# Kernel optimization log

Hardware: AMD Instinct MI355X
Metric: run time of the kernel (lower is better)

The kernel has to match this reference:

```python
import jax, jax.numpy as jnp
import numpy as np

B, S, D, H = 4, 2048, 1024, 16
W = D // H  # head width = 64


def setup_inputs() -> dict:
    key = jax.random.key(0)
    ks = jax.random.split(key, 7)
    sc = 0.02
    return {
        "x": jax.random.normal(ks[0], (B, S, D), dtype=jnp.float32),
        "mask": jnp.ones((B, S), dtype=jnp.int32),
        "Wq": jax.random.normal(ks[1], (D, D), dtype=jnp.float32) * sc,
        "bq": jax.random.normal(ks[2], (D,), dtype=jnp.float32) * sc,
        "Wk": jax.random.normal(ks[3], (D, D), dtype=jnp.float32) * sc,
        "bk": jax.random.normal(ks[4], (D,), dtype=jnp.float32) * sc,
        "Wv": jax.random.normal(ks[5], (D, D), dtype=jnp.float32) * sc,
        "bv": jax.random.normal(ks[6], (D,), dtype=jnp.float32) * sc,
    }


def reference(x, mask, Wq, bq, Wk, bk, Wv, bv):
    # Linear projections (torch Linear: y = x @ W.T + b)
    q = x @ Wq.T + bq  # (B,S,D)
    k = x @ Wk.T + bk
    v = x @ Wv.T + bv
    # split D -> (H, W) and move heads forward: (B,H,S,W)
    def split(t):
        return t.reshape(B, S, H, W).transpose(0, 2, 1, 3)
    q, k, v = split(q), split(k), split(v)
    scale = 1.0 / np.sqrt(W).astype(np.float32)
    scores = jnp.einsum("bhsw,bhtw->bhst", q, k) * scale  # (B,H,S,S)
    m = mask[:, None, None, :].astype(scores.dtype)  # (B,1,1,S)
    scores = scores - 10000.0 * (1.0 - m)
    probs = jax.nn.softmax(scores, axis=-1)  # dropout p=0.0 -> identity
    h = jnp.einsum("bhst,bhtw->bhsw", probs, v)  # (B,H,S,W)
    h = h.transpose(0, 2, 1, 3).reshape(B, S, D)  # merge heads
    return h
```

## Files before the change

### kernel.cpp

```cpp
#include <hip/hip_runtime.h>
#include <hip/hip_bf16.h>


#define NB 4
#define NS 2048
#define ND 1024
#define NH 16
#define NW 64

typedef __bf16 bf16;
typedef __bf16 bf16x2 __attribute__((ext_vector_type(2)));
typedef __bf16 bf16x4 __attribute__((ext_vector_type(4)));
typedef __bf16 bf16x8 __attribute__((ext_vector_type(8)));
typedef float f32x4 __attribute__((ext_vector_type(4)));
typedef float f32x16 __attribute__((ext_vector_type(16)));
typedef unsigned u32x4 __attribute__((ext_vector_type(4)));

__device__ __forceinline__ void gld_lds16(const void* g, void* l) {
  __builtin_amdgcn_global_load_lds(
      (const __attribute__((address_space(1))) void*)g,
      (__attribute__((address_space(3))) void*)l, 16, 0, 0);
}

__device__ __forceinline__ unsigned pack2(float lo, float hi) {
  bf16x2 t;
  t[0] = (bf16)lo;
  t[1] = (bf16)hi;
  return __builtin_bit_cast(unsigned, t);
}

__global__ void cast_f32_bf16(const float* __restrict__ src,
                              bf16* __restrict__ dst, int n) {
  int i = (blockIdx.x * blockDim.x + threadIdx.x) * 8;
  int stride = gridDim.x * blockDim.x * 8;
  for (; i < n; i += stride) {
    float4 a = *reinterpret_cast<const float4*>(src + i);
    float4 b = *reinterpret_cast<const float4*>(src + i + 4);
    bf16x8 o;
    o[0] = (bf16)a.x; o[1] = (bf16)a.y; o[2] = (bf16)a.z; o[3] = (bf16)a.w;
    o[4] = (bf16)b.x; o[5] = (bf16)b.y; o[6] = (bf16)b.z; o[7] = (bf16)b.w;
    *reinterpret_cast<bf16x8*>(dst + i) = o;
  }
}

__global__ void cast_weights(const float* __restrict__ a,
                             const float* __restrict__ b,
                             const float* __restrict__ c,
                             bf16* __restrict__ dst) {
  const int n = ND * ND;
  const int which = blockIdx.y;
  const float* src = (which == 0) ? a : ((which == 1) ? b : c);
  bf16* d = dst + (size_t)which * n;
  int i = (blockIdx.x * blockDim.x + threadIdx.x) * 8;
  float4 u = *reinterpret_cast<const float4*>(src + i);
  float4 v = *reinterpret_cast<const float4*>(src + i + 4);
  bf16x8 o;
  o[0] = (bf16)u.x; o[1] = (bf16)u.y; o[2] = (bf16)u.z; o[3] = (bf16)u.w;
  o[4] = (bf16)v.x; o[5] = (bf16)v.y; o[6] = (bf16)v.z; o[7] = (bf16)v.w;
  *reinterpret_cast<bf16x8*>(d + i) = o;
}

__global__ void mask_to_bf16(const int* __restrict__ mask,
                             bf16* __restrict__ mb, int n) {
  int i = blockIdx.x * blockDim.x + threadIdx.x;
  if (i < n) mb[i] = (bf16)(mask[i] ? 1.0f : 0.0f);
}

__global__ __launch_bounds__(256) void proj_kernel(
    const bf16* __restrict__ xb,
    const bf16* __restrict__ wq,
    const bf16* __restrict__ wk,
    const bf16* __restrict__ wv,
    const float* __restrict__ bq,
    const float* __restrict__ bk,
    const float* __restrict__ bv,
    const int* __restrict__ mask,
    bf16* __restrict__ qh,
    bf16* __restrict__ kh,
    bf16* __restrict__ vt) {
  const int mode = blockIdx.z;
  const bf16* wmat = (mode == 0) ? wq : ((mode == 1) ? wk : wv);
  const float* bias = (mode == 0) ? bq : ((mode == 1) ? bk : bv);

  __shared__ alignas(16) bf16 a_lds[128][64];
  __shared__ alignas(16) bf16 b_lds[128][64];

  const int tid = threadIdx.x;
  const int wave = tid >> 6;
  const int lane = tid & 63;
  const int wr = wave >> 1, wc = wave & 1;
  const int m0 = blockIdx.x * 128;
  const int n0 = blockIdx.y * 128;

  f32x4 acc[4][4] = {};

  const int srow = tid >> 3;
  const int scol = (tid & 7) * 8;
  const int sw_scol = scol ^ ((srow & 7) << 3);
  const int xr = (lane & 7) << 3;
  const int lr = lane & 15;
  const int g = lane >> 4;
  const int kq = g * 8;

  for (int k0 = 0; k0 < 1024; k0 += 64) {
#pragma unroll
    for (int c = 0; c < 4; ++c) {
      int row = srow + c * 32;
      gld_lds16(xb + (size_t)(m0 + row) * 1024 + k0 + sw_scol, &a_lds[row][scol]);
      gld_lds16(wmat + (size_t)(n0 + row) * 1024 + k0 + sw_scol, &b_lds[row][scol]);
    }
    __syncthreads();
#pragma unroll
    for (int kk = 0; kk < 64; kk += 32) {
      bf16x8 af[4], bfr[4];
      const int col = (kk + kq) ^ xr;
#pragma unroll
      for (int mf = 0; mf < 4; ++mf)
        af[mf] = *reinterpret_cast<const bf16x8*>(&a_lds[wr * 64 + mf * 16 + lr][col]);
#pragma unroll
      for (int nf = 0; nf < 4; ++nf)
        bfr[nf] = *reinterpret_cast<const bf16x8*>(&b_lds[wc * 64 + nf * 16 + lr][col]);
      if (mode == 2) {
#pragma unroll
        for (int mf = 0; mf < 4; ++mf)
#pragma unroll
          for (int nf = 0; nf < 4; ++nf)
            acc[mf][nf] = __builtin_amdgcn_mfma_f32_16x16x32_bf16(af[mf], bfr[nf], acc[mf][nf], 0, 0, 0);
      } else {
#pragma unroll
        for (int nf = 0; nf < 4; ++nf)
#pragma unroll
          for (int mf = 0; mf < 4; ++mf)
            acc[nf][mf] = __builtin_amdgcn_mfma_f32_16x16x32_bf16(bfr[nf], af[mf], acc[nf][mf], 0, 0, 0);
      }
    }
    __syncthreads();
  }

  if (mode == 2) {
    float msk[4][4];
#pragma unroll
    for (int mf = 0; mf < 4; ++mf) {
      const int i0 = m0 + wr * 64 + mf * 16 + g * 4;
      const int b = i0 >> 11, s = i0 & 2047;
      const int4 mm = *reinterpret_cast<const int4*>(mask + b * NS + s);
      msk[mf][0] = mm.x ? 1.f : 0.f;
      msk[mf][1] = mm.y ? 1.f : 0.f;
      msk[mf][2] = mm.z ? 1.f : 0.f;
      msk[mf][3] = mm.w ? 1.f : 0.f;
    }
#pragma unroll
    for (int nf = 0; nf < 4; ++nf) {
      const int j = n0 + wc * 64 + nf * 16 + lr;
      const float bj = bias[j];
      const int h = j >> 6, w = j & 63;
#pragma unroll
      for (int mf = 0; mf < 4; ++mf) {
        const int i0 = m0 + wr * 64 + mf * 16 + g * 4;
        const int b = i0 >> 11, s = i0 & 2047;
        bf16x4 pk;
#pragma unroll
        for (int r = 0; r < 4; ++r)
          pk[r] = (bf16)((acc[mf][nf][r] + bj) * msk[mf][r]);
        *reinterpret_cast<bf16x4*>(&vt[(((size_t)(b * NH + h)) * NW + w) * NS + s]) = pk;
      }
    }
  } else {
    bf16* dst = (mode == 0) ? qh : kh;
    const float scl = (mode == 0) ? 0.18033688011112042f : 1.0f;
#pragma unroll
    for (int nf = 0; nf < 4; ++nf) {
      const int j0 = n0 + wc * 64 + nf * 16 + g * 4;
      const f32x4 bj = *reinterpret_cast<const f32x4*>(&bias[j0]);
      const int h = j0 >> 6, w0 = j0 & 63;
#pragma unroll
      for (int mf = 0; mf < 4; ++mf) {
        const int i = m0 + wr * 64 + mf * 16 + lr;
        const int b = i >> 11, s = i & 2047;
        bf16x4 pk;
#pragma unroll
        for (int r = 0; r < 4; ++r)
          pk[r] = (bf16)((acc[nf][mf][r] + bj[r]) * scl);
        *reinterpret_cast<bf16x4*>(&dst[(((size_t)(b * NH + h)) * NS + s) * NW + w0]) = pk;
      }
    }
  }
}

__global__ __launch_bounds__(256, 4) void attn_kernel(
    const bf16* __restrict__ qh,
    const bf16* __restrict__ kh,
    const bf16* __restrict__ vt,
    const bf16* __restrict__ mb16,
    float* __restrict__ out) {
  __shared__ alignas(16) bf16 k_lds[2][64][64];
  __shared__ alignas(16) bf16 v_lds[2][64][64];

  const int tid = threadIdx.x;
  const int wave = tid >> 6;
  const int lane = tid & 63;
  const int lq = lane & 31;
  const int hi = lane >> 5;
  const int xr = (lq & 7) << 3;

  const int p = blockIdx.x;
  const int w_id = (p & 7) * 128 + (p >> 3);
  const int bh = w_id >> 4;
  const int b = bh >> 4;
  const int q0 = (w_id & 15) * 128;
  const size_t headoff = (size_t)bh * NS * NW;

  bf16x8 qf[4];
  {
    const bf16* qp = qh + headoff + (size_t)(q0 + wave * 32 + lq) * NW + hi * 8;
#pragma unroll
    for (int m = 0; m < 4; ++m)
      qf[m] = *reinterpret_cast<const bf16x8*>(qp + m * 16);
  }

  f32x16 o0 = {}, o1 = {}, lt = {};
  const bf16* mp = mb16 + b * NS;

  const int srow = tid >> 3;
  const int scol = (tid & 7) * 8;
  const int sw_scol = scol ^ ((srow & 7) << 3);

#define STAGE(buf, kt)                                                          \
  {                                                                             \
    _Pragma("unroll") for (int c = 0; c < 2; ++c) {                             \
      const int row = srow + c * 32;                                            \
      gld_lds16(kh + headoff + (size_t)((kt) + row) * NW + sw_scol,             \
                &k_lds[buf][row][scol]);                                        \
      gld_lds16(vt + headoff + (size_t)row * NS + (kt) + sw_scol,               \
                &v_lds[buf][row][scol]);                                        \
    }                                                                           \
  }

#define EXPPACK(S, PA0, PA1)                                                    \
  {                                                                             \
    unsigned w_[8];                                                             \
    _Pragma("unroll") for (int j = 0; j < 8; ++j)                               \
        w_[j] = pack2(exp2f(S[2 * j]), exp2f(S[2 * j + 1]));                    \
    asm("v_permlane32_swap_b32 %0, %1" : "+v"(w_[0]), "+v"(w_[2]));             \
    asm("v_permlane32_swap_b32 %0, %1" : "+v"(w_[1]), "+v"(w_[3]));             \
    asm("v_permlane32_swap_b32 %0, %1" : "+v"(w_[4]), "+v"(w_[6]));             \
    asm("v_permlane32_swap_b32 %0, %1" : "+v"(w_[5]), "+v"(w_[7]));             \
    u32x4 u0 = {w_[0], w_[1], w_[2], w_[3]};                                    \
    u32x4 u1 = {w_[4], w_[5], w_[6], w_[7]};                                    \
    PA0 = __builtin_bit_cast(bf16x8, u0);                                       \
    PA1 = __builtin_bit_cast(bf16x8, u1);                                       \
  }

  STAGE(0, 0);
  __syncthreads();

  int cur = 0;
  for (int kt = 0; kt < NS; kt += 64) {
    if (kt + 64 < NS) STAGE(cur ^ 1, kt + 64);

    f32x16 s0 = {}, s1 = {};
    __builtin_amdgcn_s_setprio(1);
#pragma unroll
    for (int m = 0; m < 4; ++m) {
      const int col = (m * 16 + hi * 8) ^ xr;
      bf16x8 kf0 = *reinterpret_cast<const bf16x8*>(&k_lds[cur][lq][col]);
      s0 = __builtin_amdgcn_mfma_f32_32x32x16_bf16(kf0, qf[m], s0, 0, 0, 0);
      bf16x8 kf1 = *reinterpret_cast<const bf16x8*>(&k_lds[cur][32 + lq][col]);
      s1 = __builtin_amdgcn_mfma_f32_32x32x16_bf16(kf1, qf[m], s1, 0, 0, 0);
    }
    __builtin_amdgcn_s_setprio(0);

    bf16x8 pa0, pa1, pa2, pa3;
    EXPPACK(s0, pa0, pa1);
    EXPPACK(s1, pa2, pa3);

    const bf16* mpk = mp + kt + hi * 8;
    bf16x8 mf00 = *reinterpret_cast<const bf16x8*>(mpk);
    bf16x8 mf01 = *reinterpret_cast<const bf16x8*>(mpk + 16);
    bf16x8 mf10 = *reinterpret_cast<const bf16x8*>(mpk + 32);
    bf16x8 mf11 = *reinterpret_cast<const bf16x8*>(mpk + 48);

    __builtin_amdgcn_s_setprio(1);
    lt = __builtin_amdgcn_mfma_f32_32x32x16_bf16(pa0, mf00, lt, 0, 0, 0);
    lt = __builtin_amdgcn_mfma_f32_32x32x16_bf16(pa1, mf01, lt, 0, 0, 0);
    lt = __builtin_amdgcn_mfma_f32_32x32x16_bf16(pa2, mf10, lt, 0, 0, 0);
    lt = __builtin_amdgcn_mfma_f32_32x32x16_bf16(pa3, mf11, lt, 0, 0, 0);
#pragma unroll
    for (int G = 0; G < 2; ++G) {
      const bf16x8 a0 = G ? pa2 : pa0;
      const bf16x8 a1 = G ? pa3 : pa1;
      const int c0 = (G * 32 + hi * 8) ^ xr;
      const int c1 = (G * 32 + 16 + hi * 8) ^ xr;
      bf16x8 v00 = *reinterpret_cast<const bf16x8*>(&v_lds[cur][lq][c0]);
      o0 = __builtin_amdgcn_mfma_f32_32x32x16_bf16(a0, v00, o0, 0, 0, 0);
      bf16x8 v01 = *reinterpret_cast<const bf16x8*>(&v_lds[cur][lq][c1]);
      o0 = __builtin_amdgcn_mfma_f32_32x32x16_bf16(a1, v01, o0, 0, 0, 0);
      bf16x8 v10 = *reinterpret_cast<const bf16x8*>(&v_lds[cur][32 + lq][c0]);
      o1 = __builtin_amdgcn_mfma_f32_32x32x16_bf16(a0, v10, o1, 0, 0, 0);
      bf16x8 v11 = *reinterpret_cast<const bf16x8*>(&v_lds[cur][32 + lq][c1]);
      o1 = __builtin_amdgcn_mfma_f32_32x32x16_bf16(a1, v11, o1, 0, 0, 0);
    }
    __builtin_amdgcn_s_setprio(0);

    __syncthreads();
    cur ^= 1;
  }

  const int h = bh & 15;
  float* op = out + ((size_t)b * NS) * ND + h * NW;
#pragma unroll
  for (int r = 0; r < 16; ++r) {
    const int sq = q0 + wave * 32 + (r & 3) + 8 * (r >> 2) + 4 * hi;
    const float inv = 1.0f / lt[r];
    op[(size_t)sq * ND + lq] = o0[r] * inv;
    op[(size_t)sq * ND + 32 + lq] = o1[r] * inv;
  }
#undef STAGE
#undef EXPPACK
}

extern "C" void kernel_launch(void* const* d_in, const int* in_sizes, int n_in,
                              void* d_out, int out_size, void* d_ws, size_t ws_size,
                              hipStream_t stream) {
  const float* x = (const float*)d_in[0];
  const int* mask = (const int*)d_in[1];
  const float* Wq = (const float*)d_in[2];
  const float* bq = (const float*)d_in[3];
  const float* Wk = (const float*)d_in[4];
  const float* bk = (const float*)d_in[5];
  const float* Wv = (const float*)d_in[6];
  const float* bv = (const float*)d_in[7];
  float* out = (float*)d_out;

  char* ws = (char*)d_ws;
  bf16* wqb = (bf16*)(ws + (size_t)(0) * (1 << 20));
  bf16* wkb = (bf16*)(ws + (size_t)(2) * (1 << 20));
  bf16* wvb = (bf16*)(ws + (size_t)(4) * (1 << 20));
  bf16* qhb = (bf16*)(ws + (size_t)(6) * (1 << 20));
  bf16* khb = (bf16*)(ws + (size_t)(22) * (1 << 20));
  bf16* vtb = (bf16*)(ws + (size_t)(38) * (1 << 20));
  bf16* mb16 = (bf16*)(ws + (size_t)(54) * (1 << 20));
  bf16* xb = (bf16*)d_out;

  cast_f32_bf16<<<2048, 256, 0, stream>>>(x, xb, NB * NS * ND);
  cast_weights<<<dim3(512, 3), 256, 0, stream>>>(Wq, Wk, Wv, wqb);
  mask_to_bf16<<<32, 256, 0, stream>>>(mask, mb16, NB * NS);
  proj_kernel<<<dim3(64, 8, 3), 256, 0, stream>>>(xb, wqb, wkb, wvb, bq, bk, bv,
                                                  mask, qhb, khb, vtb);
  attn_kernel<<<1024, 256, 0, stream>>>(qhb, khb, vtb, mb16, out);
}
```

Measured before the change: 310.3 us.

## Double-buffer projection GEMM LDS, template per mode, remap blocks per XCD

The projection GEMM now double-buffers its LDS tiles, so the next K-slice's global-to-LDS loads are issued before computing on the current slice, and one barrier per iteration is removed. The kernel is templated on mode and launched three times instead of branching on blockIdx.z, and blocks are remapped so each XCD handles a contiguous group of M tiles for better L2 reuse. This doubles LDS use to 64KB per block, which may lower occupancy, and adds two extra kernel launches.

```diff
diff --git a/kernel.cpp b/kernel.cpp
--- a/kernel.cpp
+++ b/kernel.cpp
@@ -66,31 +66,25 @@
   if (i < n) mb[i] = (bf16)(mask[i] ? 1.0f : 0.0f);
 }
 
+template <int MODE>
 __global__ __launch_bounds__(256) void proj_kernel(
     const bf16* __restrict__ xb,
-    const bf16* __restrict__ wq,
-    const bf16* __restrict__ wk,
-    const bf16* __restrict__ wv,
-    const float* __restrict__ bq,
-    const float* __restrict__ bk,
-    const float* __restrict__ bv,
+    const bf16* __restrict__ wmat,
+    const float* __restrict__ bias,
     const int* __restrict__ mask,
-    bf16* __restrict__ qh,
-    bf16* __restrict__ kh,
-    bf16* __restrict__ vt) {
-  const int mode = blockIdx.z;
-  const bf16* wmat = (mode == 0) ? wq : ((mode == 1) ? wk : wv);
-  const float* bias = (mode == 0) ? bq : ((mode == 1) ? bk : bv);
-
-  __shared__ alignas(16) bf16 a_lds[128][64];
-  __shared__ alignas(16) bf16 b_lds[128][64];
+    bf16* __restrict__ dst) {
+  __shared__ alignas(16) bf16 a_lds[2][128][64];
+  __shared__ alignas(16) bf16 b_lds[2][128][64];
 
   const int tid = threadIdx.x;
   const int wave = tid >> 6;
   const int lane = tid & 63;
   const int wr = wave >> 1, wc = wave & 1;
-  const int m0 = blockIdx.x * 128;
-  const int n0 = blockIdx.y * 128;
+
+  const int p = blockIdx.x;
+  const int xcd = p & 7, q = p >> 3;
+  const int m0 = (xcd * 8 + (q & 7)) * 128;
+  const int n0 = (q >> 3) * 128;
 
   f32x4 acc[4][4] = {};
 
@@ -102,25 +96,34 @@
   const int g = lane >> 4;
   const int kq = g * 8;
 
+#define PSTAGE(buf, k0)                                                         \
+  {                                                                             \
+    _Pragma("unroll") for (int c = 0; c < 4; ++c) {                             \
+      const int row = srow + c * 32;                                            \
+      gld_lds16(xb + (size_t)(m0 + row) * 1024 + (k0) + sw_scol,                \
+                &a_lds[buf][row][scol]);                                        \
+      gld_lds16(wmat + (size_t)(n0 + row) * 1024 + (k0) + sw_scol,              \
+                &b_lds[buf][row][scol]);                                        \
+    }                                                                           \
+  }
+
+  PSTAGE(0, 0);
+  __syncthreads();
+
+  int cur = 0;
   for (int k0 = 0; k0 < 1024; k0 += 64) {
-#pragma unroll
-    for (int c = 0; c < 4; ++c) {
-      int row = srow + c * 32;
-      gld_lds16(xb + (size_t)(m0 + row) * 1024 + k0 + sw_scol, &a_lds[row][scol]);
-      gld_lds16(wmat + (size_t)(n0 + row) * 1024 + k0 + sw_scol, &b_lds[row][scol]);
-    }
-    __syncthreads();
+    if (k0 + 64 < 1024) PSTAGE(cur ^ 1, k0 + 64);
 #pragma unroll
     for (int kk = 0; kk < 64; kk += 32) {
       bf16x8 af[4], bfr[4];
       const int col = (kk + kq) ^ xr;
 #pragma unroll
       for (int mf = 0; mf < 4; ++mf)
-        af[mf] = *reinterpret_cast<const bf16x8*>(&a_lds[wr * 64 + mf * 16 + lr][col]);
+        af[mf] = *reinterpret_cast<const bf16x8*>(&a_lds[cur][wr * 64 + mf * 16 + lr][col]);
 #pragma unroll
       for (int nf = 0; nf < 4; ++nf)
-        bfr[nf] = *reinterpret_cast<const bf16x8*>(&b_lds[wc * 64 + nf * 16 + lr][col]);
-      if (mode == 2) {
+        bfr[nf] = *reinterpret_cast<const bf16x8*>(&b_lds[cur][wc * 64 + nf * 16 + lr][col]);
+      if (MODE == 2) {
 #pragma unroll
         for (int mf = 0; mf < 4; ++mf)
 #pragma unroll
@@ -135,9 +138,10 @@
       }
     }
     __syncthreads();
-  }
-
-  if (mode == 2) {
+    cur ^= 1;
+  }
+
+  if (MODE == 2) {
     float msk[4][4];
 #pragma unroll
     for (int mf = 0; mf < 4; ++mf) {
@@ -162,12 +166,11 @@
 #pragma unroll
         for (int r = 0; r < 4; ++r)
           pk[r] = (bf16)((acc[mf][nf][r] + bj) * msk[mf][r]);
-        *reinterpret_cast<bf16x4*>(&vt[(((size_t)(b * NH + h)) * NW + w) * NS + s]) = pk;
+        *reinterpret_cast<bf16x4*>(&dst[(((size_t)(b * NH + h)) * NW + w) * NS + s]) = pk;
       }
     }
   } else {
-    bf16* dst = (mode == 0) ? qh : kh;
-    const float scl = (mode == 0) ? 0.18033688011112042f : 1.0f;
+    const float scl = (MODE == 0) ? 0.18033688011112042f : 1.0f;
 #pragma unroll
     for (int nf = 0; nf < 4; ++nf) {
       const int j0 = n0 + wc * 64 + nf * 16 + g * 4;
@@ -185,6 +188,7 @@
       }
     }
   }
+#undef PSTAGE
 }
 
 __global__ __launch_bounds__(256, 4) void attn_kernel(
@@ -345,7 +349,8 @@
   cast_f32_bf16<<<2048, 256, 0, stream>>>(x, xb, NB * NS * ND);
   cast_weights<<<dim3(512, 3), 256, 0, stream>>>(Wq, Wk, Wv, wqb);
   mask_to_bf16<<<32, 256, 0, stream>>>(mask, mb16, NB * NS);
-  proj_kernel<<<dim3(64, 8, 3), 256, 0, stream>>>(xb, wqb, wkb, wvb, bq, bk, bv,
-                                                  mask, qhb, khb, vtb);
+  proj_kernel<0><<<512, 256, 0, stream>>>(xb, wqb, bq, mask, qhb);
+  proj_kernel<1><<<512, 256, 0, stream>>>(xb, wkb, bk, mask, khb);
+  proj_kernel<2><<<512, 256, 0, stream>>>(xb, wvb, bv, mask, vtb);
   attn_kernel<<<1024, 256, 0, stream>>>(qhb, khb, vtb, mb16, out);
 }
```

New measurement: 281.6 us. -9.3%, faster.

## Remap projection blocks per XCD, unify MFMA order, use fast exp2

Applied to the files above, without the earlier changes.

The projection launch changes from a 3D grid to a 1D-per-mode grid and remaps block indices so that consecutive blocks on the same XCD share weight column tiles, aiming at better L2 reuse. The V projection now uses the same MFMA operand order as Q/K, which removes the branch in the inner loop. Its transposed store becomes scalar strided bf16 writes instead of packed 4-element writes, which may cost store efficiency. The attention exp uses the hardware exp2 builtin to avoid libm range handling.

```diff
diff --git a/kernel.cpp b/kernel.cpp
--- a/kernel.cpp
+++ b/kernel.cpp
@@ -66,11 +66,9 @@
   if (i < n) mb[i] = (bf16)(mask[i] ? 1.0f : 0.0f);
 }
 
-__global__ __launch_bounds__(256) void proj_kernel(
+__global__ __launch_bounds__(256) void proj_fused(
     const bf16* __restrict__ xb,
-    const bf16* __restrict__ wq,
-    const bf16* __restrict__ wk,
-    const bf16* __restrict__ wv,
+    const bf16* __restrict__ wall,
     const float* __restrict__ bq,
     const float* __restrict__ bk,
     const float* __restrict__ bv,
@@ -78,8 +76,8 @@
     bf16* __restrict__ qh,
     bf16* __restrict__ kh,
     bf16* __restrict__ vt) {
-  const int mode = blockIdx.z;
-  const bf16* wmat = (mode == 0) ? wq : ((mode == 1) ? wk : wv);
+  const int mode = blockIdx.y;
+  const bf16* wmat = wall + (size_t)mode * ND * ND;
   const float* bias = (mode == 0) ? bq : ((mode == 1) ? bk : bv);
 
   __shared__ alignas(16) bf16 a_lds[128][64];
@@ -89,8 +87,11 @@
   const int wave = tid >> 6;
   const int lane = tid & 63;
   const int wr = wave >> 1, wc = wave & 1;
-  const int m0 = blockIdx.x * 128;
-  const int n0 = blockIdx.y * 128;
+
+  const int p = blockIdx.x;
+  const int xcd = p & 7, q = p >> 3;
+  const int m0 = (xcd * 8 + (q & 7)) * 128;
+  const int n0 = (q >> 3) * 128;
 
   f32x4 acc[4][4] = {};
 
@@ -105,7 +106,7 @@
   for (int k0 = 0; k0 < 1024; k0 += 64) {
 #pragma unroll
     for (int c = 0; c < 4; ++c) {
-      int row = srow + c * 32;
+      const int row = srow + c * 32;
       gld_lds16(xb + (size_t)(m0 + row) * 1024 + k0 + sw_scol, &a_lds[row][scol]);
       gld_lds16(wmat + (size_t)(n0 + row) * 1024 + k0 + sw_scol, &b_lds[row][scol]);
     }
@@ -120,49 +121,30 @@
 #pragma unroll
       for (int nf = 0; nf < 4; ++nf)
         bfr[nf] = *reinterpret_cast<const bf16x8*>(&b_lds[wc * 64 + nf * 16 + lr][col]);
-      if (mode == 2) {
+#pragma unroll
+      for (int nf = 0; nf < 4; ++nf)
 #pragma unroll
         for (int mf = 0; mf < 4; ++mf)
-#pragma unroll
-          for (int nf = 0; nf < 4; ++nf)
-            acc[mf][nf] = __builtin_amdgcn_mfma_f32_16x16x32_bf16(af[mf], bfr[nf], acc[mf][nf], 0, 0, 0);
-      } else {
-#pragma unroll
-        for (int nf = 0; nf < 4; ++nf)
-#pragma unroll
-          for (int mf = 0; mf < 4; ++mf)
-            acc[nf][mf] = __builtin_amdgcn_mfma_f32_16x16x32_bf16(bfr[nf], af[mf], acc[nf][mf], 0, 0, 0);
-      }
+          acc[nf][mf] = __builtin_amdgcn_mfma_f32_16x16x32_bf16(bfr[nf], af[mf], acc[nf][mf], 0, 0, 0);
     }
     __syncthreads();
   }
 
   if (mode == 2) {
-    float msk[4][4];
 #pragma unroll
     for (int mf = 0; mf < 4; ++mf) {
-      const int i0 = m0 + wr * 64 + mf * 16 + g * 4;
-      const int b = i0 >> 11, s = i0 & 2047;
-      const int4 mm = *reinterpret_cast<const int4*>(mask + b * NS + s);
-      msk[mf][0] = mm.x ? 1.f : 0.f;
-      msk[mf][1] = mm.y ? 1.f : 0.f;
-      msk[mf][2] = mm.z ? 1.f : 0.f;
-      msk[mf][3] = mm.w ? 1.f : 0.f;
-    }
-#pragma unroll
-    for (int nf = 0; nf < 4; ++nf) {
-      const int j = n0 + wc * 64 + nf * 16 + lr;
-      const float bj = bias[j];
-      const int h = j >> 6, w = j & 63;
-#pragma unroll
-      for (int mf = 0; mf < 4; ++mf) {
-        const int i0 = m0 + wr * 64 + mf * 16 + g * 4;
-        const int b = i0 >> 11, s = i0 & 2047;
-        bf16x4 pk;
+      const int i = m0 + wr * 64 + mf * 16 + lr;
+      const int b = i >> 11, s = i & 2047;
+      const float mskv = mask[b * NS + s] ? 1.f : 0.f;
+#pragma unroll
+      for (int nf = 0; nf < 4; ++nf) {
+        const int j0 = n0 + wc * 64 + nf * 16 + g * 4;
+        const f32x4 bj = *reinterpret_cast<const f32x4*>(&bias[j0]);
+        const int h = j0 >> 6, w0 = j0 & 63;
 #pragma unroll
         for (int r = 0; r < 4; ++r)
-          pk[r] = (bf16)((acc[mf][nf][r] + bj) * msk[mf][r]);
-        *reinterpret_cast<bf16x4*>(&vt[(((size_t)(b * NH + h)) * NW + w) * NS + s]) = pk;
+          vt[((size_t)(b * NH + h) * NW + w0 + r) * NS + s] =
+              (bf16)((acc[nf][mf][r] + bj[r]) * mskv);
       }
     }
   } else {
@@ -240,7 +222,8 @@
   {                                                                             \
     unsigned w_[8];                                                             \
     _Pragma("unroll") for (int j = 0; j < 8; ++j)                               \
-        w_[j] = pack2(exp2f(S[2 * j]), exp2f(S[2 * j + 1]));                    \
+        w_[j] = pack2(__builtin_amdgcn_exp2f(S[2 * j]),                         \
+                      __builtin_amdgcn_exp2f(S[2 * j + 1]));                    \
     asm("v_permlane32_swap_b32 %0, %1" : "+v"(w_[0]), "+v"(w_[2]));             \
     asm("v_permlane32_swap_b32 %0, %1" : "+v"(w_[1]), "+v"(w_[3]));             \
     asm("v_permlane32_swap_b32 %0, %1" : "+v"(w_[4]), "+v"(w_[6]));             \
@@ -333,9 +316,7 @@
   float* out = (float*)d_out;
 
   char* ws = (char*)d_ws;
-  bf16* wqb = (bf16*)(ws + (size_t)(0) * (1 << 20));
-  bf16* wkb = (bf16*)(ws + (size_t)(2) * (1 << 20));
-  bf16* wvb = (bf16*)(ws + (size_t)(4) * (1 << 20));
+  bf16* wall = (bf16*)(ws + (size_t)(0) * (1 << 20));
   bf16* qhb = (bf16*)(ws + (size_t)(6) * (1 << 20));
   bf16* khb = (bf16*)(ws + (size_t)(22) * (1 << 20));
   bf16* vtb = (bf16*)(ws + (size_t)(38) * (1 << 20));
@@ -343,9 +324,9 @@
   bf16* xb = (bf16*)d_out;
 
   cast_f32_bf16<<<2048, 256, 0, stream>>>(x, xb, NB * NS * ND);
-  cast_weights<<<dim3(512, 3), 256, 0, stream>>>(Wq, Wk, Wv, wqb);
+  cast_weights<<<dim3(512, 3), 256, 0, stream>>>(Wq, Wk, Wv, wall);
   mask_to_bf16<<<32, 256, 0, stream>>>(mask, mb16, NB * NS);
-  proj_kernel<<<dim3(64, 8, 3), 256, 0, stream>>>(xb, wqb, wkb, wvb, bq, bk, bv,
-                                                  mask, qhb, khb, vtb);
+  proj_fused<<<dim3(512, 3), 256, 0, stream>>>(xb, wall, bq, bk, bv, mask,
+                                               qhb, khb, vtb);
   attn_kernel<<<1024, 256, 0, stream>>>(qhb, khb, vtb, mb16, out);
 }
```

After: 253.9 us. -18.2%, faster.
